# Kernel optimization log

Hardware: AMD Instinct MI355X
Metric: run time of the kernel (lower is better)

Reference implementation:

```python
import jax, jax.numpy as jnp
import numpy as np

PATCH_SIZE = 14
MERGE_K = 2
HIDDEN = 1024
N_IMAGES = 8
# pixel sizes (H, W) per image; all grid dims (size // patch) are even
PIXEL_SIZES = np.array([
    [1540, 1540], [1120, 1540], [784, 1092], [1540, 868],
    [952, 952], [1260, 1708], [644, 644], [1400, 1400]
], dtype=np.int32)


def setup_inputs() -> dict:
    key = jax.random.key(0)
    k1, k2 = jax.random.split(key)
    grids = PIXEL_SIZES // PATCH_SIZE
    total_tokens = int((grids[:, 0] * grids[:, 1]).sum())  # 59808
    image_features = jax.random.normal(k1, (total_tokens, HIDDEN), dtype=jnp.float32)
    # merging_layer kernel: [in_features, out_features] = [k^2 * d, d], no bias
    W = jax.random.normal(k2, (MERGE_K * MERGE_K * HIDDEN, HIDDEN), dtype=jnp.float32) * 0.02
    image_sizes = jnp.asarray(PIXEL_SIZES)
    return {"image_features": image_features, "image_sizes": image_sizes, "W": W}


def _merge_tokens(image_features, sizes_np, k):
    # sizes_np: static python list of (h, w) patch-grid dims
    d = image_features.shape[-1]
    outs = []
    off = 0
    for h, w in sizes_np:
        n = h * w
        tok = jax.lax.dynamic_slice_in_dim(image_features, off, n, axis=0)  # [h*w, d]
        # [h, w, d] -> [h//k, k, w//k, k, d] -> [h//k, w//k, k, k, d] -> [(h//k)*(w//k), k*k*d]
        g = tok.reshape(h // k, k, w // k, k, d)
        g = g.transpose(0, 2, 1, 3, 4).reshape((h // k) * (w // k), k * k * d)
        outs.append(g)
        off += n
    return jnp.concatenate(outs, axis=0)


def reference(image_features, image_sizes, W):
    sizes = [(int(h) // PATCH_SIZE, int(w) // PATCH_SIZE) for h, w in np.asarray(image_sizes)]
    merged = _merge_tokens(image_features, sizes, MERGE_K)  # [sum(h*w)/k^2, k^2*d]
    return merged @ W  # [n_merged, d]
```

## Files before the change

kernel.cpp:

```cpp
#include <hip/hip_runtime.h>
#include <hip/hip_bf16.h>
#include <stdint.h>

#define M_TOTAL 14952
#define NDIM    1024
#define KDIM    4096
#define BM      128
#define BN      128
#define BK      32
#define KSTEPS  (KDIM / BK)
#define AS_STRIDE 40

typedef __bf16 bf16x8 __attribute__((ext_vector_type(8)));
typedef float  f32x4  __attribute__((ext_vector_type(4)));

__device__ __forceinline__ unsigned pack_bf16_trunc(float a, float b) {
    return (__float_as_uint(a) >> 16) | (__float_as_uint(b) & 0xFFFF0000u);
}

__global__ void repack_w_kernel(const float* __restrict__ W,
                                unsigned short* __restrict__ Wp) {
    const int nb = blockIdx.x & 7;
    const int ks = blockIdx.x >> 3;
    const int t = threadIdx.x;
    const int k = t >> 3;
    const int part = t & 7;
    const float* src = W + (size_t)(ks * BK + k) * NDIM + nb * BN + part * 16;
    unsigned short* dst = Wp + (size_t)(nb * KSTEPS + ks) * (BK * BN)
                        + (k >> 3) * (BN * 8) + (k & 7);
#pragma unroll
    for (int i = 0; i < 16; ++i) {
        unsigned u = __float_as_uint(src[i]);
        u += 0x7FFFu + ((u >> 16) & 1u);
        dst[(size_t)(part * 16 + i) * 8] = (unsigned short)(u >> 16);
    }
}

__global__ __launch_bounds__(256, 2) void merger_gemm_kernel(
    const float* __restrict__ feat,
    const unsigned short* __restrict__ Wp,
    float* __restrict__ out) {

    __shared__ __align__(16) unsigned short As[BM * AS_STRIDE];
    __shared__ __align__(16) unsigned short Bs[4 * BN * 8];

    const int t = threadIdx.x;
    const int lane = t & 63;
    const int wave = t >> 6;
    const int wave_m = (wave >> 1) * 64;
    const int wave_n = (wave & 1) * 64;
    const int m0 = blockIdx.x * BM;
    const int n0 = blockIdx.y * BN;

    const int r = t >> 1;
    const int half = t & 1;
    int m = m0 + r;
    if (m >= M_TOTAL) m = 0;

    const int merged_off[8] = {0, 3025, 5225, 6317, 8022, 9178, 11923, 12452};
    const int tok_off[8]    = {0, 12100, 20900, 25268, 32088, 36712, 47692, 49808};
    const int gw_arr[8]     = {110, 110, 78, 62, 68, 122, 46, 100};
    const int mw_arr[8]     = {55, 55, 39, 31, 34, 61, 23, 50};

    int local = 0, gw = 110, mwv = 55, toff = 0;
#pragma unroll
    for (int i = 0; i < 8; ++i) {
        if (m >= merged_off[i]) {
            local = m - merged_off[i];
            gw = gw_arr[i]; mwv = mw_arr[i]; toff = tok_off[i];
        }
    }
    const int ii = local / mwv;
    const int jj = local - ii * mwv;
    const int base = toff + 2 * ii * gw + 2 * jj;
    const float* aptr0 = feat + (size_t)base * NDIM + half * 16;
    const float* aptr1 = feat + (size_t)(base + 1) * NDIM + half * 16;
    const float* aptr2 = feat + (size_t)(base + gw) * NDIM + half * 16;
    const float* aptr3 = feat + (size_t)(base + gw + 1) * NDIM + half * 16;

    unsigned short* as_dst = &As[r * AS_STRIDE + half * 16];
    const unsigned short* wchunk = Wp + (size_t)blockIdx.y * KSTEPS * (BK * BN);

    f32x4 acc[4][4];
#pragma unroll
    for (int i = 0; i < 4; ++i)
#pragma unroll
        for (int j = 0; j < 4; ++j) {
            f32x4 z = {0.f, 0.f, 0.f, 0.f};
            acc[i][j] = z;
        }

    const int ln = lane & 15;
    const int quad = lane >> 4;

#pragma unroll
    for (int p = 0; p < 4; ++p) {
        const float* ap = (p == 0) ? aptr0 : (p == 1) ? aptr1 : (p == 2) ? aptr2 : aptr3;
        for (int ki = 0; ki < 32; ++ki) {
            const int ks = p * 32 + ki;
            const float* src = ap + ki * 32;
            float4 f0 = *(const float4*)(src + 0);
            float4 f1 = *(const float4*)(src + 4);
            float4 f2 = *(const float4*)(src + 8);
            float4 f3 = *(const float4*)(src + 12);
            uint4 p0, p1;
            p0.x = pack_bf16_trunc(f0.x, f0.y);
            p0.y = pack_bf16_trunc(f0.z, f0.w);
            p0.z = pack_bf16_trunc(f1.x, f1.y);
            p0.w = pack_bf16_trunc(f1.z, f1.w);
            p1.x = pack_bf16_trunc(f2.x, f2.y);
            p1.y = pack_bf16_trunc(f2.z, f2.w);
            p1.z = pack_bf16_trunc(f3.x, f3.y);
            p1.w = pack_bf16_trunc(f3.z, f3.w);
            *(uint4*)as_dst = p0;
            *((uint4*)as_dst + 1) = p1;

            const unsigned short* wc = wchunk + (size_t)ks * (BK * BN) + wave * 1024 + lane * 8;
            __builtin_amdgcn_global_load_lds(
                (const __attribute__((address_space(1))) unsigned int*)wc,
                (__attribute__((address_space(3))) unsigned int*)&Bs[wave * 1024], 16, 0, 0);
            __builtin_amdgcn_global_load_lds(
                (const __attribute__((address_space(1))) unsigned int*)(wc + 512),
                (__attribute__((address_space(3))) unsigned int*)&Bs[wave * 1024 + 512], 16, 0, 0);

            __syncthreads();

            bf16x8 af[4], bf[4];
#pragma unroll
            for (int mi = 0; mi < 4; ++mi)
                af[mi] = *(const bf16x8*)&As[(wave_m + mi * 16 + ln) * AS_STRIDE + quad * 8];
#pragma unroll
            for (int ni = 0; ni < 4; ++ni)
                bf[ni] = *(const bf16x8*)&Bs[quad * 1024 + (wave_n + ni * 16 + ln) * 8];
#pragma unroll
            for (int mi = 0; mi < 4; ++mi)
#pragma unroll
                for (int ni = 0; ni < 4; ++ni)
                    acc[mi][ni] = __builtin_amdgcn_mfma_f32_16x16x32_bf16(
                        af[mi], bf[ni], acc[mi][ni], 0, 0, 0);

            __syncthreads();
        }
    }

#pragma unroll
    for (int mi = 0; mi < 4; ++mi) {
#pragma unroll
        for (int rr = 0; rr < 4; ++rr) {
            const int row = m0 + wave_m + mi * 16 + quad * 4 + rr;
            if (row < M_TOTAL) {
                float* orow = out + (size_t)row * NDIM + n0 + wave_n + ln;
#pragma unroll
                for (int ni = 0; ni < 4; ++ni)
                    orow[ni * 16] = acc[mi][ni][rr];
            }
        }
    }
}

extern "C" void kernel_launch(void* const* d_in, const int* in_sizes, int n_in,
                              void* d_out, int out_size, void* d_ws, size_t ws_size,
                              hipStream_t stream) {
    const float* feat = (const float*)d_in[0];
    const float* W = (const float*)d_in[2];
    float* out = (float*)d_out;
    unsigned short* Wp = (unsigned short*)d_ws;

    repack_w_kernel<<<1024, 256, 0, stream>>>(W, Wp);
    dim3 grid((M_TOTAL + BM - 1) / BM, NDIM / BN);
    merger_gemm_kernel<<<grid, 256, 0, stream>>>(feat, Wp, out);
}
```

Before: 602.2 us.

## Pre-gather merged activations into bf16 tiled workspace before GEMM

Adds a separate gather kernel that converts the merged 2x2 patch tokens to bf16 once and writes them into a tile-major workspace layout. The GEMM then streams both A and W tiles with direct global-to-LDS loads. Previously every N-block re-read fp32 features and converted them per tile. The W repack is also rewritten for coalesced reads with vectorized stores, and A now uses round-to-nearest instead of truncation. The cost is an extra kernel launch and roughly 120MB of workspace traffic, with the old fused path kept as a fallback when the workspace is too small.

```diff
diff --git a/kernel.cpp b/kernel.cpp
--- a/kernel.cpp
+++ b/kernel.cpp
@@ -9,11 +9,20 @@
 #define BN      128
 #define BK      32
 #define KSTEPS  (KDIM / BK)
+#define MBLKS   117
 #define AS_STRIDE 40
 
 typedef __bf16 bf16x8 __attribute__((ext_vector_type(8)));
 typedef float  f32x4  __attribute__((ext_vector_type(4)));
 
+__device__ __forceinline__ unsigned short bf16_rne(float f) {
+    unsigned u = __float_as_uint(f);
+    u += 0x7FFFu + ((u >> 16) & 1u);
+    return (unsigned short)(u >> 16);
+}
+__device__ __forceinline__ unsigned pack2_rne(float a, float b) {
+    return (unsigned)bf16_rne(a) | ((unsigned)bf16_rne(b) << 16);
+}
 __device__ __forceinline__ unsigned pack_bf16_trunc(float a, float b) {
     return (__float_as_uint(a) >> 16) | (__float_as_uint(b) & 0xFFFF0000u);
 }
@@ -23,16 +32,144 @@
     const int nb = blockIdx.x & 7;
     const int ks = blockIdx.x >> 3;
     const int t = threadIdx.x;
-    const int k = t >> 3;
-    const int part = t & 7;
-    const float* src = W + (size_t)(ks * BK + k) * NDIM + nb * BN + part * 16;
-    unsigned short* dst = Wp + (size_t)(nb * KSTEPS + ks) * (BK * BN)
-                        + (k >> 3) * (BN * 8) + (k & 7);
-#pragma unroll
-    for (int i = 0; i < 16; ++i) {
-        unsigned u = __float_as_uint(src[i]);
-        u += 0x7FFFu + ((u >> 16) & 1u);
-        dst[(size_t)(part * 16 + i) * 8] = (unsigned short)(u >> 16);
+    const int n = t & 127;
+    const int kqh = t >> 7;
+    unsigned short* chunk = Wp + (size_t)(nb * KSTEPS + ks) * (BK * BN);
+#pragma unroll
+    for (int kq2 = 0; kq2 < 2; ++kq2) {
+        const int kq = kqh * 2 + kq2;
+        const float* src = W + (size_t)(ks * 32 + kq * 8) * NDIM + nb * 128 + n;
+        float f[8];
+#pragma unroll
+        for (int k7 = 0; k7 < 8; ++k7) f[k7] = src[(size_t)k7 * NDIM];
+        uint4 pk;
+        pk.x = pack2_rne(f[0], f[1]);
+        pk.y = pack2_rne(f[2], f[3]);
+        pk.z = pack2_rne(f[4], f[5]);
+        pk.w = pack2_rne(f[6], f[7]);
+        *(uint4*)(chunk + kq * 1024 + n * 8) = pk;
+    }
+}
+
+__global__ void gather_a_kernel(const float* __restrict__ feat,
+                                unsigned short* __restrict__ Aw) {
+    const int p = blockIdx.x;
+    const int mb = blockIdx.y;
+    const int t = threadIdx.x;
+    const int mloc = t >> 1;
+    const int half = t & 1;
+    int m = mb * 128 + mloc;
+    if (m >= M_TOTAL) m = 0;
+
+    const int merged_off[8] = {0, 3025, 5225, 6317, 8022, 9178, 11923, 12452};
+    const int tok_off[8]    = {0, 12100, 20900, 25268, 32088, 36712, 47692, 49808};
+    const int gw_arr[8]     = {110, 110, 78, 62, 68, 122, 46, 100};
+    const int mw_arr[8]     = {55, 55, 39, 31, 34, 61, 23, 50};
+    int local = 0, gw = 110, mwv = 55, toff = 0;
+#pragma unroll
+    for (int i = 0; i < 8; ++i)
+        if (m >= merged_off[i]) {
+            local = m - merged_off[i];
+            gw = gw_arr[i]; mwv = mw_arr[i]; toff = tok_off[i];
+        }
+    const int ii = local / mwv;
+    const int jj = local - ii * mwv;
+    const int srcrow = toff + 2 * ii * gw + 2 * jj + (p >> 1) * gw + (p & 1);
+
+    const float* src = feat + (size_t)srcrow * NDIM + half * 512;
+    unsigned short* dst = Aw + (((size_t)(mb * 128 + p * 32 + half * 16)) << 12)
+                        + mloc * 8;
+#pragma unroll 4
+    for (int c8 = 0; c8 < 64; ++c8) {
+        float4 f0 = *(const float4*)(src + c8 * 8);
+        float4 f1 = *(const float4*)(src + c8 * 8 + 4);
+        uint4 pk;
+        pk.x = pack2_rne(f0.x, f0.y);
+        pk.y = pack2_rne(f0.z, f0.w);
+        pk.z = pack2_rne(f1.x, f1.y);
+        pk.w = pack2_rne(f1.z, f1.w);
+        *(uint4*)(dst + (size_t)c8 * 1024) = pk;
+    }
+}
+
+__global__ __launch_bounds__(256, 2) void gemm2_kernel(
+    const unsigned short* __restrict__ Aw,
+    const unsigned short* __restrict__ Wp,
+    float* __restrict__ out) {
+
+    __shared__ __align__(16) unsigned short As[4096];
+    __shared__ __align__(16) unsigned short Bs[4096];
+
+    const int t = threadIdx.x;
+    const int lane = t & 63;
+    const int wave = t >> 6;
+    const int wave_m = (wave >> 1) * 64;
+    const int wave_n = (wave & 1) * 64;
+    const int nb = blockIdx.x;
+    const int mb = blockIdx.y;
+
+    const unsigned short* achunk = Aw + ((size_t)mb * 128) * 4096 + wave * 1024 + lane * 8;
+    const unsigned short* wchunk = Wp + ((size_t)nb * 128) * 4096 + wave * 1024 + lane * 8;
+
+    const int ln = lane & 15;
+    const int quad = lane >> 4;
+
+    f32x4 acc[4][4];
+#pragma unroll
+    for (int i = 0; i < 4; ++i)
+#pragma unroll
+        for (int j = 0; j < 4; ++j) {
+            f32x4 z = {0.f, 0.f, 0.f, 0.f};
+            acc[i][j] = z;
+        }
+
+    for (int ks = 0; ks < KSTEPS; ++ks) {
+        const unsigned short* asrc = achunk + (size_t)ks * 4096;
+        const unsigned short* bsrc = wchunk + (size_t)ks * 4096;
+        __builtin_amdgcn_global_load_lds(
+            (const __attribute__((address_space(1))) unsigned int*)asrc,
+            (__attribute__((address_space(3))) unsigned int*)&As[wave * 1024], 16, 0, 0);
+        __builtin_amdgcn_global_load_lds(
+            (const __attribute__((address_space(1))) unsigned int*)(asrc + 512),
+            (__attribute__((address_space(3))) unsigned int*)&As[wave * 1024 + 512], 16, 0, 0);
+        __builtin_amdgcn_global_load_lds(
+            (const __attribute__((address_space(1))) unsigned int*)bsrc,
+            (__attribute__((address_space(3))) unsigned int*)&Bs[wave * 1024], 16, 0, 0);
+        __builtin_amdgcn_global_load_lds(
+            (const __attribute__((address_space(1))) unsigned int*)(bsrc + 512),
+            (__attribute__((address_space(3))) unsigned int*)&Bs[wave * 1024 + 512], 16, 0, 0);
+
+        __syncthreads();
+
+        bf16x8 af[4], bf[4];
+#pragma unroll
+        for (int mi = 0; mi < 4; ++mi)
+            af[mi] = *(const bf16x8*)&As[quad * 1024 + (wave_m + mi * 16 + ln) * 8];
+#pragma unroll
+        for (int ni = 0; ni < 4; ++ni)
+            bf[ni] = *(const bf16x8*)&Bs[quad * 1024 + (wave_n + ni * 16 + ln) * 8];
+#pragma unroll
+        for (int mi = 0; mi < 4; ++mi)
+#pragma unroll
+            for (int ni = 0; ni < 4; ++ni)
+                acc[mi][ni] = __builtin_amdgcn_mfma_f32_16x16x32_bf16(
+                    af[mi], bf[ni], acc[mi][ni], 0, 0, 0);
+
+        __syncthreads();
+    }
+
+#pragma unroll
+    for (int mi = 0; mi < 4; ++mi) {
+#pragma unroll
+        for (int rr = 0; rr < 4; ++rr) {
+            const int row = mb * BM + wave_m + mi * 16 + quad * 4 + rr;
+            if (row < M_TOTAL) {
+                float* orow = out + (size_t)row * NDIM + nb * BN + wave_n + ln;
+#pragma unroll
+                for (int ni = 0; ni < 4; ++ni)
+                    orow[ni * 16] = acc[mi][ni][rr];
+            }
+        }
     }
 }
 
@@ -164,9 +301,19 @@
     const float* feat = (const float*)d_in[0];
     const float* W = (const float*)d_in[2];
     float* out = (float*)d_out;
-    unsigned short* Wp = (unsigned short*)d_ws;
-
-    repack_w_kernel<<<1024, 256, 0, stream>>>(W, Wp);
-    dim3 grid((M_TOTAL + BM - 1) / BM, NDIM / BN);
-    merger_gemm_kernel<<<grid, 256, 0, stream>>>(feat, Wp, out);
-}
+
+    const size_t A_BYTES = (size_t)MBLKS * 128 * 8192;
+    const size_t W_BYTES = (size_t)8 * KSTEPS * 8192;
+
+    if (ws_size >= A_BYTES + W_BYTES) {
+        unsigned short* Aw = (unsigned short*)d_ws;
+        unsigned short* Wp = (unsigned short*)((char*)d_ws + A_BYTES);
+        repack_w_kernel<<<1024, 256, 0, stream>>>(W, Wp);
+        gather_a_kernel<<<dim3(4, MBLKS), 256, 0, stream>>>(feat, Aw);
+        gemm2_kernel<<<dim3(8, MBLKS), 256, 0, stream>>>(Aw, Wp, out);
+    } else {
+        unsigned short* Wp = (unsigned short*)d_ws;
+        repack_w_kernel<<<1024, 256, 0, stream>>>(W, Wp);
+        merger_gemm_kernel<<<dim3(MBLKS, 8), 256, 0, stream>>>(feat, Wp, out);
+    }
+}
```

Result: faster. 546.1 us (-9.3%).
